# Kernel optimization log

Measured on AMD Instinct MI355X. Metric: run time of the kernel, lower is better.

The kernel has to match this reference:

```python
import jax, jax.numpy as jnp
import numpy as np

D_MODEL = 1024
N_HEADS = 16
D_K = D_MODEL // N_HEADS
B, L = 8, 512


def setup_inputs() -> dict:
    key = jax.random.key(0)
    ks = jax.random.split(key, 12)
    s = 0.02
    return {
        "q": jax.random.normal(ks[0], (B, L, D_MODEL), jnp.float32),
        "k": jax.random.normal(ks[1], (B, L, D_MODEL), jnp.float32),
        "v": jax.random.normal(ks[2], (B, L, D_MODEL), jnp.float32),
        "rel_pos_emb": jax.random.normal(ks[3], (L, L, D_MODEL), jnp.float32) * s,
        "mask": jnp.ones((1, 1, L, L), jnp.int32),
        "Wq": jax.random.normal(ks[4], (D_MODEL, D_MODEL), jnp.float32) * s,
        "bq": jnp.zeros((D_MODEL,), jnp.float32),
        "Wk": jax.random.normal(ks[5], (D_MODEL, D_MODEL), jnp.float32) * s,
        "bk": jnp.zeros((D_MODEL,), jnp.float32),
        "Wv": jax.random.normal(ks[6], (D_MODEL, D_MODEL), jnp.float32) * s,
        "bv": jnp.zeros((D_MODEL,), jnp.float32),
        "Wo": jax.random.normal(ks[7], (D_MODEL, D_MODEL), jnp.float32) * s,
        "bo": jnp.zeros((D_MODEL,), jnp.float32),
    }


def reference(q, k, v, rel_pos_emb, mask, Wq, bq, Wk, bk, Wv, bv, Wo, bo):
    Bn, Ln, D = q.shape
    H, dk = N_HEADS, D // N_HEADS
    # QKV projections (nn.Linear: x @ W^T + b), split heads -> [B,H,L,dk]
    qh = (q @ Wq.T + bq).reshape(Bn, Ln, H, dk).transpose(0, 2, 1, 3)
    kh = (k @ Wk.T + bk).reshape(Bn, Ln, H, dk).transpose(0, 2, 1, 3)
    vh = (v @ Wv.T + bv).reshape(Bn, Ln, H, dk).transpose(0, 2, 1, 3)
    # relative position embeddings -> [H,L,L,dk]
    rel = rel_pos_emb.reshape(Ln, Ln, H, dk).transpose(2, 0, 1, 3)
    scale = 1.0 / jnp.sqrt(jnp.float32(dk))
    scores = jnp.einsum('bhld,bhrd->bhlr', qh, kh) * scale
    scores = scores + jnp.einsum('bhld,hlrd->bhlr', qh, rel)
    scores = jnp.where(mask == 0, jnp.float32(-1e9), scores)
    attn = jax.nn.softmax(scores, axis=-1)  # dropout omitted (eval mode)
    out = jnp.einsum('bhlr,bhrd->bhld', attn, vh)
    out = out.transpose(0, 2, 1, 3).reshape(Bn, Ln, D)
    return out @ Wo.T + bo
```

## Files before the change

kernel.cpp:

```cpp
#include <hip/hip_runtime.h>

typedef __attribute__((ext_vector_type(8))) short short8;
typedef __attribute__((ext_vector_type(4))) float f32x4;
typedef __attribute__((ext_vector_type(4))) unsigned short u16x4;
typedef unsigned int u32;
typedef unsigned short ushort_t;

union frag_u { u32 w[4]; short8 s; };

static __device__ __forceinline__ unsigned short f2bf(float x) {
  union { float f; unsigned u; } v; v.f = x;
  unsigned r = v.u + 0x7fffu + ((v.u >> 16) & 1u);
  return (unsigned short)(r >> 16);
}
static __device__ __forceinline__ float bf2f(unsigned short h) {
  union { unsigned u; float f; } v; v.u = ((unsigned)h) << 16;
  return v.f;
}
static __device__ __forceinline__ u32 pk_bf16(float a, float b) {
  u32 r;
  asm("v_cvt_pk_bf16_f32 %0, %1, %2" : "=v"(r) : "v"(a), "v"(b));
  return r;
}

static __device__ __forceinline__ void barrier_lds() {
  __builtin_amdgcn_sched_barrier(0);
  asm volatile("s_waitcnt lgkmcnt(0)" ::: "memory");
  __builtin_amdgcn_s_barrier();
  __builtin_amdgcn_sched_barrier(0);
}

static __device__ __forceinline__ void gl_lds16(const void* g, void* s) {
  __builtin_amdgcn_global_load_lds(
      (const __attribute__((address_space(1))) void*)g,
      (__attribute__((address_space(3))) void*)s, 16, 0, 0);
}

__global__ __launch_bounds__(256) void to_bf16_3(const float* __restrict__ s0,
                                                 const float* __restrict__ s1,
                                                 const float* __restrict__ s2,
                                                 ushort_t* __restrict__ dst,
                                                 int lg2, int n4) {
  int i = blockIdx.x * blockDim.x + threadIdx.x;
  int stride = gridDim.x * blockDim.x;
  for (; i < n4; i += stride) {
    int which = i >> lg2;
    const float* s = which == 0 ? s0 : which == 1 ? s1 : s2;
    int local = i - (which << lg2);
    float4 x = *(const float4*)&s[(size_t)local * 4];
    u16x4 o;
    o.x = f2bf(x.x); o.y = f2bf(x.y); o.z = f2bf(x.z); o.w = f2bf(x.w);
    *(u16x4*)&dst[(size_t)i * 4] = o;
  }
}

__global__ __launch_bounds__(256) void split3_bf16(const float* __restrict__ src,
                                                   ushort_t* __restrict__ dst, int n) {
  int i = blockIdx.x * blockDim.x + threadIdx.x;
  int stride = gridDim.x * blockDim.x;
  for (; i < n; i += stride) {
    int r = i >> 10, c = i & 1023;
    float x = src[i];
    unsigned short hi = f2bf(x);
    unsigned short lo = f2bf(x - bf2f(hi));
    ushort_t* row = dst + (size_t)r * 3072;
    row[c] = hi; row[1024 + c] = hi; row[2048 + c] = lo;
  }
}

__global__ __launch_bounds__(256) void gemm_qkv(
    const ushort_t* __restrict__ qbf, const ushort_t* __restrict__ kbf,
    const ushort_t* __restrict__ vbf, const ushort_t* __restrict__ Wqb,
    const ushort_t* __restrict__ Wkb, const ushort_t* __restrict__ Wvb,
    const float* __restrict__ bq, const float* __restrict__ bk,
    const float* __restrict__ bv, ushort_t* __restrict__ qhb,
    ushort_t* __restrict__ khb, ushort_t* __restrict__ vT) {
  __shared__ ushort_t As[2][128 * 32];
  __shared__ ushort_t Bs[2][128 * 32];
  const int t = threadIdx.x;
  const int lane = t & 63;
  const int w = t >> 6;
  const int wr = w >> 1, wc = w & 1;
  const int bid = blockIdx.x;
  const int mt = bid / 24, ntg = bid % 24;
  const int which = ntg >> 3, nt = ntg & 7;
  const ushort_t* A  = which == 0 ? qbf : which == 1 ? kbf : vbf;
  const ushort_t* Bw = which == 0 ? Wqb : which == 1 ? Wkb : Wvb;
  const float* bias  = which == 0 ? bq  : which == 1 ? bk  : bv;
  const int m0 = mt * 128, n0 = nt * 128;
  const int r16 = lane & 15, kb = lane >> 4;

  f32x4 acc[4][4];
#pragma unroll
  for (int mi = 0; mi < 4; ++mi)
#pragma unroll
    for (int ni = 0; ni < 4; ++ni) acc[mi][ni] = (f32x4){0.f, 0.f, 0.f, 0.f};

  auto STAGE = [&](int buf, int k0) {
#pragma unroll
    for (int i = 0; i < 2; ++i) {
      int c = i * 256 + t;
      int row = c >> 2, kc = (c & 3) * 8;
      gl_lds16(&A[(size_t)(m0 + row) * 1024 + k0 + kc], &As[buf][c * 8]);
      gl_lds16(&Bw[(size_t)(n0 + row) * 1024 + k0 + kc], &Bs[buf][c * 8]);
    }
  };

  STAGE(0, 0);
  __syncthreads();
  int cur = 0;
  for (int kt = 0; kt < 32; ++kt) {
    if (kt + 1 < 32) STAGE(cur ^ 1, (kt + 1) * 32);
    short8 af[4], bf[4];
#pragma unroll
    for (int mi = 0; mi < 4; ++mi)
      af[mi] = *(const short8*)&As[cur][(wr * 64 + mi * 16 + r16) * 32 + kb * 8];
#pragma unroll
    for (int ni = 0; ni < 4; ++ni)
      bf[ni] = *(const short8*)&Bs[cur][(wc * 64 + ni * 16 + r16) * 32 + kb * 8];
#pragma unroll
    for (int mi = 0; mi < 4; ++mi)
#pragma unroll
      for (int ni = 0; ni < 4; ++ni)
        acc[mi][ni] = __builtin_amdgcn_mfma_f32_16x16x32_bf16(af[mi], bf[ni], acc[mi][ni], 0, 0, 0);
    __syncthreads();
    cur ^= 1;
  }

  const int rowD = (lane >> 4) * 4;
#pragma unroll
  for (int mi = 0; mi < 4; ++mi) {
#pragma unroll
    for (int ni = 0; ni < 4; ++ni) {
      int n = n0 + wc * 64 + ni * 16 + (lane & 15);
      float bv4 = bias[n];
      int mbase = m0 + wr * 64 + mi * 16 + rowD;
      float vals[4];
#pragma unroll
      for (int j = 0; j < 4; ++j) vals[j] = acc[mi][ni][j] + bv4;
      int hh = n >> 6, d = n & 63;
      if (which == 0) {
#pragma unroll
        for (int j = 0; j < 4; ++j) {
          int m = mbase + j;
          int b = m >> 9, l = m & 511;
          qhb[(((size_t)(b * 16 + hh)) * 512 + l) * 64 + d] = f2bf(vals[j]);
        }
      } else if (which == 1) {
#pragma unroll
        for (int j = 0; j < 4; ++j) {
          int m = mbase + j;
          int b = m >> 9, r = m & 511;
          khb[(((size_t)(b * 16 + hh)) * 512 + r) * 64 + d] = f2bf(vals[j]);
        }
      } else {
        int b = mbase >> 9, r = mbase & 511;
        u16x4 pkv;
        pkv.x = f2bf(vals[0]); pkv.y = f2bf(vals[1]);
        pkv.z = f2bf(vals[2]); pkv.w = f2bf(vals[3]);
        *(u16x4*)&vT[(((size_t)(b * 16 + hh)) * 64 + d) * 512 + r] = pkv;
      }
    }
  }
}

__global__ __launch_bounds__(256) void gemm_out(const ushort_t* __restrict__ A,
                                                const ushort_t* __restrict__ Bw,
                                                const float* __restrict__ bias,
                                                float* __restrict__ Cout) {
  __shared__ ushort_t As[2][128 * 32];
  __shared__ ushort_t Bs[2][128 * 32];
  const int t = threadIdx.x;
  const int lane = t & 63;
  const int w = t >> 6;
  const int wr = w >> 1, wc = w & 1;
  const int mt = blockIdx.x >> 3, nt = blockIdx.x & 7;
  const int m0 = mt * 128, n0 = nt * 128;
  const int r16 = lane & 15, kb = lane >> 4;

  f32x4 acc[4][4];
#pragma unroll
  for (int mi = 0; mi < 4; ++mi)
#pragma unroll
    for (int ni = 0; ni < 4; ++ni) acc[mi][ni] = (f32x4){0.f, 0.f, 0.f, 0.f};

  auto STAGE = [&](int buf, int k0) {
#pragma unroll
    for (int i = 0; i < 2; ++i) {
      int c = i * 256 + t;
      int row = c >> 2, kc = (c & 3) * 8;
      gl_lds16(&A[(size_t)(m0 + row) * 3072 + k0 + kc], &As[buf][c * 8]);
      gl_lds16(&Bw[(size_t)(n0 + row) * 3072 + k0 + kc], &Bs[buf][c * 8]);
    }
  };

  STAGE(0, 0);
  __syncthreads();
  int cur = 0;
  for (int kt = 0; kt < 96; ++kt) {
    if (kt + 1 < 96) STAGE(cur ^ 1, (kt + 1) * 32);
    short8 af[4], bf[4];
#pragma unroll
    for (int mi = 0; mi < 4; ++mi)
      af[mi] = *(const short8*)&As[cur][(wr * 64 + mi * 16 + r16) * 32 + kb * 8];
#pragma unroll
    for (int ni = 0; ni < 4; ++ni)
      bf[ni] = *(const short8*)&Bs[cur][(wc * 64 + ni * 16 + r16) * 32 + kb * 8];
#pragma unroll
    for (int mi = 0; mi < 4; ++mi)
#pragma unroll
      for (int ni = 0; ni < 4; ++ni)
        acc[mi][ni] = __builtin_amdgcn_mfma_f32_16x16x32_bf16(af[mi], bf[ni], acc[mi][ni], 0, 0, 0);
    __syncthreads();
    cur ^= 1;
  }

  const int rowD = (lane >> 4) * 4;
#pragma unroll
  for (int mi = 0; mi < 4; ++mi) {
#pragma unroll
    for (int ni = 0; ni < 4; ++ni) {
      int n = n0 + wc * 64 + ni * 16 + (lane & 15);
      float bv = bias[n];
      int mbase = m0 + wr * 64 + mi * 16 + rowD;
#pragma unroll
      for (int j = 0; j < 4; ++j)
        Cout[(size_t)(mbase + j) * 1024 + n] = acc[mi][ni][j] + bv;
    }
  }
}

__global__ __launch_bounds__(256, 2) void attn_mfma(
    const ushort_t* __restrict__ qhb, const ushort_t* __restrict__ khb,
    const ushort_t* __restrict__ vT, const float* __restrict__ rel,
    const int* __restrict__ mask, ushort_t* __restrict__ Abig) {
  __shared__ ushort_t qs[8][16][64];
  __shared__ float sp2[2][8][17][20];
  const int t = threadIdx.x;
  const int w = t >> 6, lane = t & 63, lh = lane & 15, lg = lane >> 4;
  const int bid = blockIdx.x;
  const int slot = bid & 7, grp = bid >> 3;
  const int h = slot * 2 + (grp & 1);
  const int l0 = (grp >> 1) * 16;
  const int b0 = w * 2;
  const int off = (grp * 5) & 31;

  {
    int idx = t * 32;
    int b = idx >> 10, l = (idx >> 6) & 15, d0 = idx & 63;
    const ushort_t* src = &qhb[(((size_t)(b * 16 + h)) * 512 + l0 + l) * 64 + d0];
    int xr = (l & 7) ^ b;
#pragma unroll
    for (int jj = 0; jj < 4; ++jj) {
      short8 vq = *(const short8*)&src[jj * 8];
      int pos = ((d0 >> 3) + jj) ^ xr;
      *(short8*)&qs[b][l][pos * 8] = vq;
    }
  }

  f32x4 R[16];
  const float* relbase = &rel[(size_t)(l0 + w * 4) * 512 * 1024 + h * 64 + lg * 8];
  auto LOAD_REL = [&](int r0_) {
#pragma unroll
    for (int li = 0; li < 4; ++li) {
      const float* rp = relbase + ((size_t)li * 512 + r0_ + lh) * 1024;
#pragma unroll
      for (int kb = 0; kb < 2; ++kb) {
        R[li * 4 + kb * 2 + 0] = *(const f32x4*)&rp[kb * 32];
        R[li * 4 + kb * 2 + 1] = *(const f32x4*)&rp[kb * 32 + 4];
      }
    }
  };
  LOAD_REL(off * 16);

  f32x4 O[2][4];
#pragma unroll
  for (int i = 0; i < 2; ++i)
#pragma unroll
    for (int j = 0; j < 4; ++j) O[i][j] = (f32x4){0.f, 0.f, 0.f, 0.f};
  float m_run[2] = {-1e30f, -1e30f}, s_run[2] = {0.f, 0.f};

  __syncthreads();

#pragma unroll 1
  for (int it = 0; it < 32; ++it) {
    const int r0 = ((it + off) & 31) * 16;
    const int cur = it & 1;

    short8 kf[2][2], vf[2][4];
#pragma unroll
    for (int bh = 0; bh < 2; ++bh) {
#pragma unroll
      for (int kb = 0; kb < 2; ++kb)
        kf[bh][kb] = *(const short8*)&khb[(((size_t)((b0 + bh) * 16 + h)) * 512 + r0 + lh) * 64 + kb * 32 + lg * 8];
#pragma unroll
      for (int dt = 0; dt < 4; ++dt)
        vf[bh][dt] = *(const short8*)&vT[(((size_t)((b0 + bh) * 16 + h)) * 64 + dt * 16 + lh) * 512 + r0 + lg * 8];
    }
    int4 mk = *(const int4*)&mask[(size_t)(l0 + lh) * 512 + r0 + lg * 4];

#pragma unroll
    for (int li = 0; li < 4; ++li) {
      frag_u a0, a1;
      f32x4 v00 = R[li * 4 + 0], v01 = R[li * 4 + 1];
      f32x4 v10 = R[li * 4 + 2], v11 = R[li * 4 + 3];
      a0.w[0] = pk_bf16(v00[0], v00[1]); a0.w[1] = pk_bf16(v00[2], v00[3]);
      a0.w[2] = pk_bf16(v01[0], v01[1]); a0.w[3] = pk_bf16(v01[2], v01[3]);
      a1.w[0] = pk_bf16(v10[0], v10[1]); a1.w[1] = pk_bf16(v10[2], v10[3]);
      a1.w[2] = pk_bf16(v11[0], v11[1]); a1.w[3] = pk_bf16(v11[2], v11[3]);
      int l = w * 4 + li;
      int xr2 = (l & 7) ^ (lh & 7);
      short8 q0 = *(const short8*)&qs[lh & 7][l][(lg ^ xr2) * 8];
      short8 q1 = *(const short8*)&qs[lh & 7][l][((4 + lg) ^ xr2) * 8];
      f32x4 acc = (f32x4){0.f, 0.f, 0.f, 0.f};
      acc = __builtin_amdgcn_mfma_f32_16x16x32_bf16(a0.s, q0, acc, 0, 0, 0);
      acc = __builtin_amdgcn_mfma_f32_16x16x32_bf16(a1.s, q1, acc, 0, 0, 0);
      if (lh < 8) *(f32x4*)&sp2[cur][lh][l][lg * 4] = acc;
    }
    if (it < 31) LOAD_REL(((it + 1 + off) & 31) * 16);

    barrier_lds();

    __builtin_amdgcn_s_setprio(1);
#pragma unroll
    for (int bh = 0; bh < 2; ++bh) {
      int xqk = (lh & 7) ^ (b0 + bh);
      short8 qb0 = *(const short8*)&qs[b0 + bh][lh][(lg ^ xqk) * 8];
      short8 qb1 = *(const short8*)&qs[b0 + bh][lh][((4 + lg) ^ xqk) * 8];
      f32x4 s1 = (f32x4){0.f, 0.f, 0.f, 0.f};
      s1 = __builtin_amdgcn_mfma_f32_16x16x32_bf16(kf[bh][0], qb0, s1, 0, 0, 0);
      s1 = __builtin_amdgcn_mfma_f32_16x16x32_bf16(kf[bh][1], qb1, s1, 0, 0, 0);
      f32x4 s2 = *(const f32x4*)&sp2[cur][b0 + bh][lh][lg * 4];
      f32x4 S;
      S[0] = (mk.x == 0) ? -1e9f : (s1[0] * 0.125f + s2[0]);
      S[1] = (mk.y == 0) ? -1e9f : (s1[1] * 0.125f + s2[1]);
      S[2] = (mk.z == 0) ? -1e9f : (s1[2] * 0.125f + s2[2]);
      S[3] = (mk.w == 0) ? -1e9f : (s1[3] * 0.125f + s2[3]);
      float mt = fmaxf(fmaxf(S[0], S[1]), fmaxf(S[2], S[3]));
      mt = fmaxf(mt, __shfl_xor(mt, 16));
      mt = fmaxf(mt, __shfl_xor(mt, 32));
      float mn = fmaxf(m_run[bh], mt);
      float fsc = __expf(m_run[bh] - mn);
      f32x4 P;
      P[0] = __expf(S[0] - mn); P[1] = __expf(S[1] - mn);
      P[2] = __expf(S[2] - mn); P[3] = __expf(S[3] - mn);
      float ps = P[0] + P[1] + P[2] + P[3];
      ps += __shfl_xor(ps, 16);
      ps += __shfl_xor(ps, 32);
      s_run[bh] = s_run[bh] * fsc + ps;
      m_run[bh] = mn;
#pragma unroll
      for (int dt = 0; dt < 4; ++dt) O[bh][dt] *= fsc;
      u32 pk0 = pk_bf16(P[0], P[1]), pk1 = pk_bf16(P[2], P[3]);
      int s0l = (lh + 32 * lg) & 63;
      u32 w0 = (u32)__shfl((int)pk0, s0l), w1 = (u32)__shfl((int)pk1, s0l);
      u32 w2 = (u32)__shfl((int)pk0, s0l + 16), w3 = (u32)__shfl((int)pk1, s0l + 16);
      bool vld = (lg < 2);
      frag_u pb;
      pb.w[0] = vld ? w0 : 0u; pb.w[1] = vld ? w1 : 0u;
      pb.w[2] = vld ? w2 : 0u; pb.w[3] = vld ? w3 : 0u;
#pragma unroll
      for (int dt = 0; dt < 4; ++dt)
        O[bh][dt] = __builtin_amdgcn_mfma_f32_16x16x32_bf16(vf[bh][dt], pb.s, O[bh][dt], 0, 0, 0);
    }
    __builtin_amdgcn_s_setprio(0);
  }

#pragma unroll
  for (int bh = 0; bh < 2; ++bh) {
    float inv = 1.0f / s_run[bh];
    ushort_t* rowp = &Abig[(size_t)((b0 + bh) * 512 + l0 + lh) * 3072];
#pragma unroll
    for (int dt = 0; dt < 4; ++dt) {
      int c = h * 64 + dt * 16 + lg * 4;
      f32x4 o = O[bh][dt];
      float x0 = o[0] * inv, x1 = o[1] * inv, x2 = o[2] * inv, x3 = o[3] * inv;
      u16x4 hi, lo;
      hi.x = f2bf(x0); lo.x = f2bf(x0 - bf2f(hi.x));
      hi.y = f2bf(x1); lo.y = f2bf(x1 - bf2f(hi.y));
      hi.z = f2bf(x2); lo.z = f2bf(x2 - bf2f(hi.z));
      hi.w = f2bf(x3); lo.w = f2bf(x3 - bf2f(hi.w));
      *(u16x4*)&rowp[c] = hi;
      *(u16x4*)&rowp[1024 + c] = lo;
      *(u16x4*)&rowp[2048 + c] = hi;
    }
  }
}

extern "C" void kernel_launch(void* const* d_in, const int* in_sizes, int n_in,
                              void* d_out, int out_size, void* d_ws, size_t ws_size,
                              hipStream_t stream) {
  const float* q    = (const float*)d_in[0];
  const float* k    = (const float*)d_in[1];
  const float* v    = (const float*)d_in[2];
  const float* rel  = (const float*)d_in[3];
  const int*   mask = (const int*)d_in[4];
  const float* Wq   = (const float*)d_in[5];
  const float* bq   = (const float*)d_in[6];
  const float* Wk   = (const float*)d_in[7];
  const float* bk   = (const float*)d_in[8];
  const float* Wv   = (const float*)d_in[9];
  const float* bv   = (const float*)d_in[10];
  const float* Wo   = (const float*)d_in[11];
  const float* bo   = (const float*)d_in[12];
  float* out = (float*)d_out;

  char* ws = (char*)d_ws;
  ushort_t* qhb = (ushort_t*)(ws);
  ushort_t* khb = (ushort_t*)(ws + 16777216);
  ushort_t* vT  = (ushort_t*)(ws + 16777216 + 8388608);
  ushort_t* X   = (ushort_t*)(ws + 33554432);
  ushort_t* Y   = (ushort_t*)(ws + 58720256);
  ushort_t* qbf = X;
  ushort_t* kbf = X + 4194304;
  ushort_t* vbf = X + 8388608;
  ushort_t* Wqb = Y;
  ushort_t* Wkb = Y + 1048576;
  ushort_t* Wvb = Y + 2097152;

  to_bf16_3<<<1536, 256, 0, stream>>>(q, k, v, X, 20, 3145728);
  to_bf16_3<<<384, 256, 0, stream>>>(Wq, Wk, Wv, Y, 18, 786432);

  gemm_qkv<<<768, 256, 0, stream>>>(qbf, kbf, vbf, Wqb, Wkb, Wvb,
                                    bq, bk, bv, qhb, khb, vT);

  split3_bf16<<<1024, 256, 0, stream>>>(Wo, Y, 1048576);

  attn_mfma<<<512, 256, 0, stream>>>(qhb, khb, vT, rel, mask, X);

  gemm_out<<<256, 256, 0, stream>>>(X, Y, bo, out);
}
```

Measured before the change: 446.9 us.

## Stream relative-position tiles into double-buffered LDS via direct global-to-LDS loads

The rel_pos_emb tile prefetch moves from 16 f32x4 registers per lane into a double-buffered LDS area, filled with global_load_lds DMA. Reads use an XOR swizzle against bank conflicts, and an explicit vmcnt wait keeps the next tile's DMA in flight during compute. The aim is to free registers and keep the large, bandwidth-bound rel stream overlapped with the MFMA work. In exchange, the 128KB LDS buffer cuts occupancy to one block per CU (launch bounds changed from 2 to 1). Each iteration also gains an extra barrier, and sp2 becomes single-buffered.

```diff
diff --git a/kernel.cpp b/kernel.cpp
--- a/kernel.cpp
+++ b/kernel.cpp
@@ -26,6 +26,11 @@
 static __device__ __forceinline__ void barrier_lds() {
   __builtin_amdgcn_sched_barrier(0);
   asm volatile("s_waitcnt lgkmcnt(0)" ::: "memory");
+  __builtin_amdgcn_s_barrier();
+  __builtin_amdgcn_sched_barrier(0);
+}
+static __device__ __forceinline__ void barrier_plain() {
+  __builtin_amdgcn_sched_barrier(0);
   __builtin_amdgcn_s_barrier();
   __builtin_amdgcn_sched_barrier(0);
 }
@@ -230,14 +235,16 @@
   }
 }
 
-__global__ __launch_bounds__(256, 2) void attn_mfma(
+__global__ __launch_bounds__(256, 1) void attn_mfma(
     const ushort_t* __restrict__ qhb, const ushort_t* __restrict__ khb,
     const ushort_t* __restrict__ vT, const float* __restrict__ rel,
     const int* __restrict__ mask, ushort_t* __restrict__ Abig) {
+  __shared__ float relL[2][16][16][64];
   __shared__ ushort_t qs[8][16][64];
-  __shared__ float sp2[2][8][17][20];
+  __shared__ float sp2[8][17][20];
   const int t = threadIdx.x;
   const int w = t >> 6, lane = t & 63, lh = lane & 15, lg = lane >> 4;
+  const int w4 = w * 4;
   const int bid = blockIdx.x;
   const int slot = bid & 7, grp = bid >> 3;
   const int h = slot * 2 + (grp & 1);
@@ -258,20 +265,20 @@
     }
   }
 
-  f32x4 R[16];
-  const float* relbase = &rel[(size_t)(l0 + w * 4) * 512 * 1024 + h * 64 + lg * 8];
-  auto LOAD_REL = [&](int r0_) {
-#pragma unroll
-    for (int li = 0; li < 4; ++li) {
-      const float* rp = relbase + ((size_t)li * 512 + r0_ + lh) * 1024;
-#pragma unroll
-      for (int kb = 0; kb < 2; ++kb) {
-        R[li * 4 + kb * 2 + 0] = *(const f32x4*)&rp[kb * 32];
-        R[li * 4 + kb * 2 + 1] = *(const f32x4*)&rp[kb * 32 + 4];
-      }
+  const int rdel = lane >> 4;
+  const int blk = lane & 15;
+  auto DMA_REL = [&](int buf, int r0_) {
+#pragma unroll
+    for (int j = 0; j < 16; ++j) {
+      const int li = j >> 2;
+      const int rr4 = (j & 3) * 4;
+      const int r_local = rr4 + rdel;
+      const int blkp = blk ^ (r_local & 7);
+      const float* src = rel +
+          ((size_t)(l0 + w4 + li) * 512 + r0_ + r_local) * 1024 + h * 64 + blkp * 4;
+      gl_lds16(src, &relL[buf][w4 + li][rr4][0]);
     }
   };
-  LOAD_REL(off * 16);
 
   f32x4 O[2][4];
 #pragma unroll
@@ -281,6 +288,7 @@
   float m_run[2] = {-1e30f, -1e30f}, s_run[2] = {0.f, 0.f};
 
   __syncthreads();
+  DMA_REL(0, off * 16);
 
 #pragma unroll 1
   for (int it = 0; it < 32; ++it) {
@@ -299,25 +307,40 @@
     }
     int4 mk = *(const int4*)&mask[(size_t)(l0 + lh) * 512 + r0 + lg * 4];
 
+    __builtin_amdgcn_sched_barrier(0);
+    DMA_REL(cur ^ 1, (((it + 1 + off) & 31)) * 16);
+    __builtin_amdgcn_sched_barrier(0);
+    asm volatile("s_waitcnt vmcnt(16)" ::: "memory");
+    __builtin_amdgcn_sched_barrier(0);
+
 #pragma unroll
     for (int li = 0; li < 4; ++li) {
+      const int l = w4 + li;
+      const float* row = &relL[cur][l][lh][0];
+      const int s = lh & 7;
       frag_u a0, a1;
-      f32x4 v00 = R[li * 4 + 0], v01 = R[li * 4 + 1];
-      f32x4 v10 = R[li * 4 + 2], v11 = R[li * 4 + 3];
-      a0.w[0] = pk_bf16(v00[0], v00[1]); a0.w[1] = pk_bf16(v00[2], v00[3]);
-      a0.w[2] = pk_bf16(v01[0], v01[1]); a0.w[3] = pk_bf16(v01[2], v01[3]);
-      a1.w[0] = pk_bf16(v10[0], v10[1]); a1.w[1] = pk_bf16(v10[2], v10[3]);
-      a1.w[2] = pk_bf16(v11[0], v11[1]); a1.w[3] = pk_bf16(v11[2], v11[3]);
-      int l = w * 4 + li;
+      {
+        int bb = lg * 2;
+        f32x4 Ra = *(const f32x4*)(row + ((bb ^ s) * 4));
+        f32x4 Rb = *(const f32x4*)(row + (((bb + 1) ^ s) * 4));
+        a0.w[0] = pk_bf16(Ra[0], Ra[1]); a0.w[1] = pk_bf16(Ra[2], Ra[3]);
+        a0.w[2] = pk_bf16(Rb[0], Rb[1]); a0.w[3] = pk_bf16(Rb[2], Rb[3]);
+      }
+      {
+        int bb = 8 + lg * 2;
+        f32x4 Ra = *(const f32x4*)(row + ((bb ^ s) * 4));
+        f32x4 Rb = *(const f32x4*)(row + (((bb + 1) ^ s) * 4));
+        a1.w[0] = pk_bf16(Ra[0], Ra[1]); a1.w[1] = pk_bf16(Ra[2], Ra[3]);
+        a1.w[2] = pk_bf16(Rb[0], Rb[1]); a1.w[3] = pk_bf16(Rb[2], Rb[3]);
+      }
       int xr2 = (l & 7) ^ (lh & 7);
       short8 q0 = *(const short8*)&qs[lh & 7][l][(lg ^ xr2) * 8];
       short8 q1 = *(const short8*)&qs[lh & 7][l][((4 + lg) ^ xr2) * 8];
       f32x4 acc = (f32x4){0.f, 0.f, 0.f, 0.f};
       acc = __builtin_amdgcn_mfma_f32_16x16x32_bf16(a0.s, q0, acc, 0, 0, 0);
       acc = __builtin_amdgcn_mfma_f32_16x16x32_bf16(a1.s, q1, acc, 0, 0, 0);
-      if (lh < 8) *(f32x4*)&sp2[cur][lh][l][lg * 4] = acc;
-    }
-    if (it < 31) LOAD_REL(((it + 1 + off) & 31) * 16);
+      if (lh < 8) *(f32x4*)&sp2[lh][l][lg * 4] = acc;
+    }
 
     barrier_lds();
 
@@ -330,7 +353,7 @@
       f32x4 s1 = (f32x4){0.f, 0.f, 0.f, 0.f};
       s1 = __builtin_amdgcn_mfma_f32_16x16x32_bf16(kf[bh][0], qb0, s1, 0, 0, 0);
       s1 = __builtin_amdgcn_mfma_f32_16x16x32_bf16(kf[bh][1], qb1, s1, 0, 0, 0);
-      f32x4 s2 = *(const f32x4*)&sp2[cur][b0 + bh][lh][lg * 4];
+      f32x4 s2 = *(const f32x4*)&sp2[b0 + bh][lh][lg * 4];
       f32x4 S;
       S[0] = (mk.x == 0) ? -1e9f : (s1[0] * 0.125f + s2[0]);
       S[1] = (mk.y == 0) ? -1e9f : (s1[1] * 0.125f + s2[1]);
@@ -364,6 +387,8 @@
         O[bh][dt] = __builtin_amdgcn_mfma_f32_16x16x32_bf16(vf[bh][dt], pb.s, O[bh][dt], 0, 0, 0);
     }
     __builtin_amdgcn_s_setprio(0);
+
+    barrier_plain();
   }
 
 #pragma unroll
```

Result: slower. 481.4 us (+7.7%).
